# Kernel tuning notes

Hardware: AMD Instinct MI355X
Metric: run time of the kernel (lower is better)

The kernel has to match this reference:

```python
import jax, jax.numpy as jnp
import numpy as np

B, N, DIM = 1, 512, 1024
HEADS, DH = 16, 64          # dim_head = 64, _dim = heads*dh = 1024
P = 32                      # projection_dim
P2 = P // 2
NEG_INF = -1e30


def setup_inputs() -> dict:
    key = jax.random.key(0)
    ks = jax.random.split(key, 14)
    s = 0.02
    _dim = HEADS * DH
    return {
        "x":    jax.random.normal(ks[0], (B, N, DIM), dtype=jnp.float32),
        "Wqkv": jax.random.normal(ks[1], (3 * _dim, DIM), dtype=jnp.float32) * s,
        "Wout": jax.random.normal(ks[2], (DIM, _dim), dtype=jnp.float32) * s,
        "Wq":   jax.random.normal(ks[3], (P, DH), dtype=jnp.float32) * s,
        "bq":   jax.random.normal(ks[4], (P,), dtype=jnp.float32) * s,
        "Wk":   jax.random.normal(ks[5], (P, DH), dtype=jnp.float32) * s,
        "bk":   jax.random.normal(ks[6], (P,), dtype=jnp.float32) * s,
        "W1":   jax.random.normal(ks[7], (P, 2 * P), dtype=jnp.float32) * s,
        "b1":   jax.random.normal(ks[8], (P,), dtype=jnp.float32) * s,
        "W2":   jax.random.normal(ks[9], (P2, P), dtype=jnp.float32) * s,
        "b2":   jax.random.normal(ks[10], (P2,), dtype=jnp.float32) * s,
        "W3":   jax.random.normal(ks[11], (1, P2), dtype=jnp.float32) * s,
        "b3":   jax.random.normal(ks[12], (1,), dtype=jnp.float32) * s,
    }


def reference(x, Wqkv, Wout, Wq, bq, Wk, bk, W1, b1, W2, b2, W3, b3):
    b, n, _ = x.shape
    # qkv projection, then einops 'b n (d k h) -> k b h n d' split (d outermost!)
    qkv = jnp.einsum('bnc,oc->bno', x, Wqkv).reshape(b, n, DH, 3, HEADS)
    q = jnp.transpose(qkv[:, :, :, 0, :], (0, 3, 1, 2))  # [b,h,n,dh]
    k = jnp.transpose(qkv[:, :, :, 1, :], (0, 3, 1, 2))
    v = jnp.transpose(qkv[:, :, :, 2, :], (0, 3, 1, 2))

    qp = jnp.einsum('bhnd,pd->bhnp', q, Wq) + bq  # [b,h,n,P]
    kp = jnp.einsum('bhnd,pd->bhnp', k, Wk) + bk

    # linear1 on concat(q_i, k_j): split W1 -> broadcast-add (same math,
    # avoids materializing the [b,h,n,n,2P] concat tensor)
    W1q, W1k = W1[:, :P], W1[:, P:]
    a = jnp.einsum('bhnp,qp->bhnq', qp, W1q)      # [b,h,n,P]
    c = jnp.einsum('bhnp,qp->bhnq', kp, W1k)      # [b,h,n,P]
    h1 = jax.nn.relu(a[:, :, :, None, :] + c[:, :, None, :, :] + b1)  # [b,h,n,n,P]
    h2 = jax.nn.relu(jnp.einsum('bhijp,qp->bhijq', h1, W2) + b2)      # [b,h,n,n,P/2]
    score = jnp.einsum('bhijq,oq->bhijo', h2, W3)[..., 0] + b3[0]     # [b,h,n,n]

    # causal mask (triu(1) filled with -inf)
    i = jnp.arange(n)
    causal = i[None, :] > i[:, None]
    score = jnp.where(causal, NEG_INF, score)

    attn = jax.nn.softmax(score, axis=-1)
    out = jnp.einsum('bhij,bhjd->bhid', attn, v)                      # [b,h,n,dh]
    out = jnp.transpose(out, (0, 2, 1, 3)).reshape(b, n, HEADS * DH)  # b n (h d)
    return jnp.einsum('bne,oe->bno', out, Wout)
```

## Files before the change

### kernel.cpp

```cpp
#include <hip/hip_runtime.h>
#include <hip/hip_bf16.h>
#include <hip/hip_fp16.h>
#include <math.h>

#define N_SEQ 512
#define DIM   1024
#define HEADS 16
#define DH    64
#define P     32
#define P2    16
#define PSTR  520

typedef short    bf16x8 __attribute__((ext_vector_type(8)));
typedef _Float16 f16x8  __attribute__((ext_vector_type(8)));
typedef float    f32x4  __attribute__((ext_vector_type(4)));

__device__ inline unsigned short f2bf(float f) {
  union { float f; unsigned u; } v; v.f = f;
  unsigned r = (v.u + 0x7fffu + ((v.u >> 16) & 1u)) >> 16;
  return (unsigned short)r;
}

union H8 { f16x8 v; __half2 h2[4]; unsigned u32[4]; };

__global__ __launch_bounds__(256) void prep(
    const float* __restrict__ Wqkv, const float* __restrict__ Wq,
    const float* __restrict__ bq, const float* __restrict__ Wk,
    const float* __restrict__ bk, const float* __restrict__ W1,
    const float* __restrict__ x, const float* __restrict__ Wout,
    short* __restrict__ Wcomb, short* __restrict__ xb,
    short* __restrict__ Woutb, float* __restrict__ ba32,
    float* __restrict__ bc32) {
  const int b = blockIdx.x, tid = threadIdx.x;
  if (b < 256) {
    __shared__ float W1s[32][33];
    __shared__ float Wqs[32][65];
    __shared__ float wsm[32][65];
    __shared__ __align__(16) float qs[64][132];
    const int part = b >> 7, rem = b & 127;
    const int h = rem >> 3, c0 = (rem & 7) * 128;
    const int grow = part * 16 + h;
    for (int idx = tid; idx < 1024; idx += 256)
      W1s[idx >> 5][idx & 31] = W1[(idx >> 5) * 64 + part * 32 + (idx & 31)];
    const float* Wsel = part ? Wk : Wq;
    for (int idx = tid; idx < 2048; idx += 256)
      Wqs[idx >> 6][idx & 63] = Wsel[idx];
    for (int idx = tid; idx < 2048; idx += 256) {
      const int d = idx >> 5, c4 = idx & 31;
      *(float4*)&qs[d][c4 * 4] =
          *(const float4*)(Wqkv + (size_t)(d * 48 + grow) * DIM + c0 + c4 * 4);
    }
    __syncthreads();
    for (int idx = tid; idx < 2048; idx += 256) {
      const int q = idx >> 6, d = idx & 63;
      float s = 0.f;
#pragma unroll
      for (int p = 0; p < 32; ++p) s += W1s[q][p] * Wqs[p][d];
      wsm[q][d] = s;
    }
    __syncthreads();
    for (int idx = tid; idx < 4096; idx += 256) {
      const int q = idx >> 7, c = idx & 127;
      float s = 0.f;
#pragma unroll
      for (int d = 0; d < 64; ++d) s += wsm[q][d] * qs[d][c];
      Wcomb[(size_t)(part * 512 + h * 32 + q) * DIM + c0 + c] = (short)f2bf(s);
    }
    if (rem == 0 && tid < 32) {
      const float* bsel = part ? bk : bq;
      float s = 0.f;
#pragma unroll
      for (int p = 0; p < 32; ++p) s += W1s[tid][p] * bsel[p];
      (part ? bc32 : ba32)[tid] = s;
    }
  } else if (b < 384) {
#pragma unroll
    for (int rr = 0; rr < 8; ++rr) {
      const int ov = (b - 256) * 8 + rr;
      const int h = ov >> 6, d = ov & 63;
      const float4 v = *(const float4*)(Wqkv + (size_t)(d * 48 + 32 + h) * DIM + tid * 4);
      ushort4 o;
      o.x = f2bf(v.x); o.y = f2bf(v.y); o.z = f2bf(v.z); o.w = f2bf(v.w);
      *(ushort4*)(Wcomb + (size_t)(1024 + ov) * DIM + tid * 4) = o;
    }
  } else if (b < 512) {
    const int idx = (b - 384) * 256 + tid;
#pragma unroll
    for (int u = 0; u < 4; ++u) {
      const int t = u * 32768 + idx;
      const float4 v = ((const float4*)x)[t];
      ushort4 o;
      o.x = f2bf(v.x); o.y = f2bf(v.y); o.z = f2bf(v.z); o.w = f2bf(v.w);
      ((ushort4*)xb)[t] = o;
    }
  } else {
    const int idx = (b - 512) * 256 + tid;
#pragma unroll
    for (int u = 0; u < 4; ++u) {
      const int t = u * 65536 + idx;
      const float4 v = ((const float4*)Wout)[t];
      ushort4 o;
      o.x = f2bf(v.x); o.y = f2bf(v.y); o.z = f2bf(v.z); o.w = f2bf(v.w);
      ((ushort4*)Woutb)[t] = o;
    }
  }
}

__global__ __launch_bounds__(256) void gemm_acv(
    const short* __restrict__ xb, const short* __restrict__ Wcomb,
    const float* __restrict__ ba32, const float* __restrict__ bc32,
    const float* __restrict__ b1,
    __half* __restrict__ a_buf, __half* __restrict__ cb_buf,
    __half* __restrict__ vT) {
  const int wave = blockIdx.x * 4 + (threadIdx.x >> 6);
  const int tm = wave >> 6;
  const int tn = wave & 63;
  const int lane = threadIdx.x & 63;
  const int m = lane & 15;
  const int quad = lane >> 4;

  const short* pa  = xb + (size_t)(tm * 16 + m) * DIM + quad * 8;
  const short* pb0 = Wcomb + (size_t)(tn * 32 + m) * DIM + quad * 8;
  const short* pb1 = pb0 + (size_t)16 * DIM;

  f32x4 acc0 = {0.f,0.f,0.f,0.f}, acc1 = {0.f,0.f,0.f,0.f};
#pragma unroll 4
  for (int k = 0; k < DIM; k += 32) {
    const bf16x8 av = *(const bf16x8*)(pa + k);
    const bf16x8 b0 = *(const bf16x8*)(pb0 + k);
    const bf16x8 b1v = *(const bf16x8*)(pb1 + k);
    acc0 = __builtin_amdgcn_mfma_f32_16x16x32_bf16(av, b0, acc0, 0, 0, 0);
    acc1 = __builtin_amdgcn_mfma_f32_16x16x32_bf16(av, b1v, acc1, 0, 0, 0);
  }

#pragma unroll
  for (int r = 0; r < 4; ++r) {
    const int n = tm * 16 + quad * 4 + r;
#pragma unroll
    for (int half = 0; half < 2; ++half) {
      const int o = tn * 32 + m + half * 16;
      const float val = half ? acc1[r] : acc0[r];
      if (o < 512) {
        const int h = o >> 5, q = o & 31;
        a_buf[((size_t)h * N_SEQ + n) * P + q] = __float2half(val + ba32[q]);
      } else if (o < 1024) {
        const int oo = o - 512, h = oo >> 5, q = oo & 31;
        cb_buf[((size_t)h * N_SEQ + n) * P + q] = __float2half(val + bc32[q] + b1[q]);
      } else {
        const int ov = o - 1024, h = ov >> 6, d = ov & 63;
        vT[((size_t)h * DH + d) * N_SEQ + n] = __float2half(val);
      }
    }
  }
}

__device__ inline float rowscore(const H8& a, const H8& c, f16x8 w2f,
                                 float4 b2q, float4 w3q) {
  H8 u;
#pragma unroll
  for (int k = 0; k < 4; ++k) {
    const __half2 s = __hadd2(a.h2[k], c.h2[k]);
    union { __half2 h; unsigned u; } cv; cv.h = s;
    const unsigned msk = (cv.u >> 15) & 0x00010001u;
    u.u32[k] = cv.u & ~(msk * 0xFFFFu);
  }
  f32x4 acc = {0.f, 0.f, 0.f, 0.f};
  acc = __builtin_amdgcn_mfma_f32_16x16x32_f16(w2f, u.v, acc, 0, 0, 0);
  return fmaxf(acc[0] + b2q.x, 0.f) * w3q.x + fmaxf(acc[1] + b2q.y, 0.f) * w3q.y
       + fmaxf(acc[2] + b2q.z, 0.f) * w3q.z + fmaxf(acc[3] + b2q.w, 0.f) * w3q.w;
}

__device__ inline float quadreduce4(float p0, float p1, float p2, float p3,
                                    int quad) {
  const float sx = (quad & 1) ? p0 : p1;
  const float sy = (quad & 1) ? p2 : p3;
  const float rx = __shfl_xor(sx, 16);
  const float ry = __shfl_xor(sy, 16);
  const float aa = ((quad & 1) ? p1 : p0) + rx;
  const float bb = ((quad & 1) ? p3 : p2) + ry;
  const float sz = (quad & 2) ? aa : bb;
  const float rz = __shfl_xor(sz, 32);
  return ((quad & 2) ? bb : aa) + rz;
}

__global__ __launch_bounds__(256) void attn_fused(
    const __half* __restrict__ a_g, const __half* __restrict__ cb_g,
    const float* __restrict__ W2, const float* __restrict__ b2,
    const float* __restrict__ W3,
    const __half* __restrict__ vT, short* __restrict__ attnb) {
  const int p = blockIdx.x;
  const int h = blockIdx.y;
  const int tid = threadIdx.x;
  const int w = tid >> 6;
  const int lane = tid & 63;
  const int m = lane & 15, quad = lane >> 4;

  __shared__ __align__(16) __half probS[32][PSTR];
  __shared__ float invS[32];

  const int tlo = p, thi = 31 - p;
  const int nlo = p + 1, nhi = 32 - p;

  {
    f16x8 w2f;
    {
      const float4* wp = (const float4*)(W2 + m * P + quad * 8);
      const float4 w0 = wp[0], w1 = wp[1];
      H8 u;
      u.h2[0] = __floats2half2_rn(w0.x, w0.y);
      u.h2[1] = __floats2half2_rn(w0.z, w0.w);
      u.h2[2] = __floats2half2_rn(w1.x, w1.y);
      u.h2[3] = __floats2half2_rn(w1.z, w1.w);
      w2f = u.v;
    }
    const float4 b2q = *(const float4*)(b2 + quad * 4);
    const float4 w3q = *(const float4*)(W3 + quad * 4);

    H8 alo[4], ahi[4];
#pragma unroll
    for (int r = 0; r < 4; ++r) {
      alo[r].v = *(const f16x8*)(a_g + ((size_t)h * N_SEQ + tlo * 16 + 4 * w + r) * P + quad * 8);
      ahi[r].v = *(const f16x8*)(a_g + ((size_t)h * N_SEQ + thi * 16 + 4 * w + r) * P + quad * 8);
    }

    for (int jt = 0; jt < nhi; ++jt) {
      H8 cb;
      cb.v = *(const f16x8*)(cb_g + ((size_t)h * N_SEQ + jt * 16 + m) * P + quad * 8);
      const float q0 = rowscore(ahi[0], cb, w2f, b2q, w3q);
      const float q1 = rowscore(ahi[1], cb, w2f, b2q, w3q);
      const float q2 = rowscore(ahi[2], cb, w2f, b2q, w3q);
      const float q3 = rowscore(ahi[3], cb, w2f, b2q, w3q);
      const float fh = quadreduce4(q0, q1, q2, q3, quad);
      probS[16 + 4 * w + quad][jt * 16 + m] = __float2half(fh);
      if (jt < nlo) {
        const float s0 = rowscore(alo[0], cb, w2f, b2q, w3q);
        const float s1 = rowscore(alo[1], cb, w2f, b2q, w3q);
        const float s2 = rowscore(alo[2], cb, w2f, b2q, w3q);
        const float s3 = rowscore(alo[3], cb, w2f, b2q, w3q);
        const float fl = quadreduce4(s0, s1, s2, s3, quad);
        probS[4 * w + quad][jt * 16 + m] = __float2half(fl);
      }
    }
  }
  __syncthreads();

  {
    const int lr = 8 * w + (lane >> 3);
    const int c  = lane & 7;
    const int gi = (lr < 16) ? (tlo * 16 + lr) : (thi * 16 + (lr - 16));
    float mx = -1e30f;
#pragma unroll
    for (int k = 0; k < 8; ++k) {
      const int c0 = k * 64 + c * 8;
      if (c0 > gi) break;
      H8 vv; vv.v = *(const f16x8*)&probS[lr][c0];
#pragma unroll
      for (int u = 0; u < 8; ++u) {
        const float s = __half2float(vv.h2[u >> 1].data[u & 1]);
        if (c0 + u <= gi) mx = fmaxf(mx, s);
      }
    }
#pragma unroll
    for (int msk = 1; msk < 8; msk <<= 1) mx = fmaxf(mx, __shfl_xor(mx, msk));
    float sum = 0.f;
#pragma unroll
    for (int k = 0; k < 8; ++k) {
      const int c0 = k * 64 + c * 8;
      H8 vv; vv.v = *(const f16x8*)&probS[lr][c0];
      H8 o;
#pragma unroll
      for (int u = 0; u < 4; ++u) {
        float e0 = 0.f, e1 = 0.f;
        if (c0 + 2 * u <= gi) {
          e0 = __expf(__half2float(vv.h2[u].data[0]) - mx);
          if (c0 + 2 * u + 1 <= gi)
            e1 = __expf(__half2float(vv.h2[u].data[1]) - mx);
        }
        sum += e0 + e1;
        o.h2[u] = __floats2half2_rn(e0, e1);
      }
      *(f16x8*)&probS[lr][c0] = o.v;
    }
#pragma unroll
    for (int msk = 1; msk < 8; msk <<= 1) sum += __shfl_xor(sum, msk);
    if (c == 0) invS[lr] = 1.f / sum;
  }
  __syncthreads();

  {
    const int d0 = w * 16;
    const __half* pb = vT + ((size_t)h * DH + d0 + m) * N_SEQ + quad * 8;
#pragma unroll
    for (int half = 0; half < 2; ++half) {
      const int lbase = half ? 16 : 0;
      const int tile = half ? thi : tlo;
      const int nk = half ? ((33 - p) >> 1) : ((p + 2) >> 1);
      f32x4 acc = {0.f, 0.f, 0.f, 0.f};
      for (int k = 0; k < nk; ++k) {
        const f16x8 a = *(const f16x8*)&probS[lbase + m][k * 32 + quad * 8];
        const f16x8 b = *(const f16x8*)(pb + k * 32);
        acc = __builtin_amdgcn_mfma_f32_16x16x32_f16(a, b, acc, 0, 0, 0);
      }
#pragma unroll
      for (int r = 0; r < 4; ++r) {
        const int lrow = quad * 4 + r;
        const float val = acc[r] * invS[lbase + lrow];
        attnb[(size_t)(tile * 16 + lrow) * DIM + h * DH + d0 + m] = (short)f2bf(val);
      }
    }
  }
}

__global__ __launch_bounds__(256) void gemm_out16(
    const short* __restrict__ A, const short* __restrict__ B,
    float* __restrict__ C) {
  const int wave = blockIdx.x * 4 + (threadIdx.x >> 6);
  const int tm = wave >> 6;
  const int tn = wave & 63;
  const int lane = threadIdx.x & 63;
  const int m = lane & 15, quad = lane >> 4;

  const short* pa = A + (size_t)(tm * 16 + m) * DIM + quad * 8;
  const short* pb = B + (size_t)(tn * 16 + m) * DIM + quad * 8;

  f32x4 acc = {0.f, 0.f, 0.f, 0.f};
#pragma unroll 4
  for (int k = 0; k < DIM; k += 32) {
    const bf16x8 a = *(const bf16x8*)(pa + k);
    const bf16x8 b = *(const bf16x8*)(pb + k);
    acc = __builtin_amdgcn_mfma_f32_16x16x32_bf16(a, b, acc, 0, 0, 0);
  }
#pragma unroll
  for (int r = 0; r < 4; ++r)
    C[(size_t)(tm * 16 + quad * 4 + r) * DIM + tn * 16 + m] = acc[r];
}

extern "C" void kernel_launch(void* const* d_in, const int* in_sizes, int n_in,
                              void* d_out, int out_size, void* d_ws, size_t ws_size,
                              hipStream_t stream) {
  const float* x    = (const float*)d_in[0];
  const float* Wqkv = (const float*)d_in[1];
  const float* Wout = (const float*)d_in[2];
  const float* Wq   = (const float*)d_in[3];
  const float* bq   = (const float*)d_in[4];
  const float* Wk   = (const float*)d_in[5];
  const float* bk   = (const float*)d_in[6];
  const float* W1   = (const float*)d_in[7];
  const float* b1   = (const float*)d_in[8];
  const float* W2   = (const float*)d_in[9];
  const float* b2   = (const float*)d_in[10];
  const float* W3   = (const float*)d_in[11];
  float* out = (float*)d_out;

  float*  ws     = (float*)d_ws;
  float*  ba32   = ws;
  float*  bc32   = ba32 + 32;
  __half* a_buf  = (__half*)(bc32 + 32);
  __half* cb_buf = a_buf + (size_t)HEADS * N_SEQ * P;
  __half* vT     = cb_buf + (size_t)HEADS * N_SEQ * P;
  short*  Wcomb  = (short*)(vT + (size_t)HEADS * DH * N_SEQ);
  short*  xb     = Wcomb + (size_t)2048 * DIM;
  short*  Woutb  = xb + (size_t)N_SEQ * DIM;
  short*  attnb  = Woutb + (size_t)DIM * DIM;

  prep<<<768, 256, 0, stream>>>(Wqkv, Wq, bq, Wk, bk, W1, x, Wout,
                                Wcomb, xb, Woutb, ba32, bc32);

  gemm_acv<<<512, 256, 0, stream>>>(xb, Wcomb, ba32, bc32, b1,
                                    a_buf, cb_buf, vT);

  dim3 g3(16, HEADS);
  attn_fused<<<g3, 256, 0, stream>>>(a_buf, cb_buf, W2, b2, W3, vT, attnb);

  gemm_out16<<<512, 256, 0, stream>>>(attnb, Woutb, out);
}
```

Before: 174.8 us.

## Register-block GEMMs to 128x128 tiles, double attention block threads, simplify rowscore

Both bf16 GEMMs switch from one 16x16/16x32 tile per wave to 64x64 register-blocked tiles per wave in 128x128 blocks. Each loaded fragment now feeds four MFMAs, cutting global load traffic per MFMA, but the grids shrink to 64 and 32 blocks on a GPU with many CUs. The attention kernel moves to 512 threads, splitting score tiles by parity across wave pairs and giving each wave a single PV half, which adds parallelism per block. Rowscore replaces the bitmask ReLU with a vector max, folds b2 into the MFMA accumulator init, and b1 is folded into bc32 during prep.

```diff
diff --git a/kernel.cpp b/kernel.cpp
--- a/kernel.cpp
+++ b/kernel.cpp
@@ -27,6 +27,7 @@
     const float* __restrict__ Wqkv, const float* __restrict__ Wq,
     const float* __restrict__ bq, const float* __restrict__ Wk,
     const float* __restrict__ bk, const float* __restrict__ W1,
+    const float* __restrict__ b1,
     const float* __restrict__ x, const float* __restrict__ Wout,
     short* __restrict__ Wcomb, short* __restrict__ xb,
     short* __restrict__ Woutb, float* __restrict__ ba32,
@@ -71,6 +72,7 @@
       float s = 0.f;
 #pragma unroll
       for (int p = 0; p < 32; ++p) s += W1s[tid][p] * bsel[p];
+      if (part) s += b1[tid];
       (part ? bc32 : ba32)[tid] = s;
     }
   } else if (b < 384) {
@@ -109,65 +111,76 @@
 __global__ __launch_bounds__(256) void gemm_acv(
     const short* __restrict__ xb, const short* __restrict__ Wcomb,
     const float* __restrict__ ba32, const float* __restrict__ bc32,
-    const float* __restrict__ b1,
     __half* __restrict__ a_buf, __half* __restrict__ cb_buf,
     __half* __restrict__ vT) {
-  const int wave = blockIdx.x * 4 + (threadIdx.x >> 6);
-  const int tm = wave >> 6;
-  const int tn = wave & 63;
+  const int bb = blockIdx.x;
+  const int tm = bb >> 4;
+  const int tn = bb & 15;
+  const int w = threadIdx.x >> 6;
+  const int wm = w >> 1, wn = w & 1;
   const int lane = threadIdx.x & 63;
-  const int m = lane & 15;
-  const int quad = lane >> 4;
-
-  const short* pa  = xb + (size_t)(tm * 16 + m) * DIM + quad * 8;
-  const short* pb0 = Wcomb + (size_t)(tn * 32 + m) * DIM + quad * 8;
-  const short* pb1 = pb0 + (size_t)16 * DIM;
-
-  f32x4 acc0 = {0.f,0.f,0.f,0.f}, acc1 = {0.f,0.f,0.f,0.f};
-#pragma unroll 4
+  const int m = lane & 15, quad = lane >> 4;
+
+  const int row0 = tm * 128 + wm * 64;
+  const int col0 = tn * 128 + wn * 64;
+
+  const short* pa = xb + (size_t)(row0 + m) * DIM + quad * 8;
+  const short* pb = Wcomb + (size_t)(col0 + m) * DIM + quad * 8;
+
+  f32x4 acc[4][4];
+#pragma unroll
+  for (int mi = 0; mi < 4; ++mi)
+#pragma unroll
+    for (int ni = 0; ni < 4; ++ni) acc[mi][ni] = (f32x4){0.f, 0.f, 0.f, 0.f};
+
+#pragma unroll 2
   for (int k = 0; k < DIM; k += 32) {
-    const bf16x8 av = *(const bf16x8*)(pa + k);
-    const bf16x8 b0 = *(const bf16x8*)(pb0 + k);
-    const bf16x8 b1v = *(const bf16x8*)(pb1 + k);
-    acc0 = __builtin_amdgcn_mfma_f32_16x16x32_bf16(av, b0, acc0, 0, 0, 0);
-    acc1 = __builtin_amdgcn_mfma_f32_16x16x32_bf16(av, b1v, acc1, 0, 0, 0);
-  }
-
-#pragma unroll
-  for (int r = 0; r < 4; ++r) {
-    const int n = tm * 16 + quad * 4 + r;
-#pragma unroll
-    for (int half = 0; half < 2; ++half) {
-      const int o = tn * 32 + m + half * 16;
-      const float val = half ? acc1[r] : acc0[r];
-      if (o < 512) {
-        const int h = o >> 5, q = o & 31;
-        a_buf[((size_t)h * N_SEQ + n) * P + q] = __float2half(val + ba32[q]);
-      } else if (o < 1024) {
-        const int oo = o - 512, h = oo >> 5, q = oo & 31;
-        cb_buf[((size_t)h * N_SEQ + n) * P + q] = __float2half(val + bc32[q] + b1[q]);
-      } else {
-        const int ov = o - 1024, h = ov >> 6, d = ov & 63;
-        vT[((size_t)h * DH + d) * N_SEQ + n] = __float2half(val);
+    bf16x8 af[4], bf[4];
+#pragma unroll
+    for (int i = 0; i < 4; ++i) {
+      af[i] = *(const bf16x8*)(pa + (size_t)i * 16 * DIM + k);
+      bf[i] = *(const bf16x8*)(pb + (size_t)i * 16 * DIM + k);
+    }
+#pragma unroll
+    for (int mi = 0; mi < 4; ++mi)
+#pragma unroll
+      for (int ni = 0; ni < 4; ++ni)
+        acc[mi][ni] = __builtin_amdgcn_mfma_f32_16x16x32_bf16(
+            af[mi], bf[ni], acc[mi][ni], 0, 0, 0);
+  }
+
+#pragma unroll
+  for (int mi = 0; mi < 4; ++mi) {
+#pragma unroll
+    for (int ni = 0; ni < 4; ++ni) {
+      const int o = col0 + ni * 16 + m;
+#pragma unroll
+      for (int r = 0; r < 4; ++r) {
+        const int n = row0 + mi * 16 + quad * 4 + r;
+        const float val = acc[mi][ni][r];
+        if (o < 512) {
+          const int hh = o >> 5, q = o & 31;
+          a_buf[((size_t)hh * N_SEQ + n) * P + q] = __float2half(val + ba32[q]);
+        } else if (o < 1024) {
+          const int oo = o - 512, hh = oo >> 5, q = oo & 31;
+          cb_buf[((size_t)hh * N_SEQ + n) * P + q] = __float2half(val + bc32[q]);
+        } else {
+          const int ov = o - 1024, hh = ov >> 6, d = ov & 63;
+          vT[((size_t)hh * DH + d) * N_SEQ + n] = __float2half(val);
+        }
       }
     }
   }
 }
 
 __device__ inline float rowscore(const H8& a, const H8& c, f16x8 w2f,
-                                 float4 b2q, float4 w3q) {
-  H8 u;
-#pragma unroll
-  for (int k = 0; k < 4; ++k) {
-    const __half2 s = __hadd2(a.h2[k], c.h2[k]);
-    union { __half2 h; unsigned u; } cv; cv.h = s;
-    const unsigned msk = (cv.u >> 15) & 0x00010001u;
-    u.u32[k] = cv.u & ~(msk * 0xFFFFu);
-  }
-  f32x4 acc = {0.f, 0.f, 0.f, 0.f};
-  acc = __builtin_amdgcn_mfma_f32_16x16x32_f16(w2f, u.v, acc, 0, 0, 0);
-  return fmaxf(acc[0] + b2q.x, 0.f) * w3q.x + fmaxf(acc[1] + b2q.y, 0.f) * w3q.y
-       + fmaxf(acc[2] + b2q.z, 0.f) * w3q.z + fmaxf(acc[3] + b2q.w, 0.f) * w3q.w;
+                                 f32x4 b2q, float4 w3q) {
+  const f16x8 z = (f16x8)(_Float16)0;
+  const f16x8 u = __builtin_elementwise_max(a.v + c.v, z);
+  f32x4 acc = b2q;
+  acc = __builtin_amdgcn_mfma_f32_16x16x32_f16(w2f, u, acc, 0, 0, 0);
+  return fmaxf(acc[0], 0.f) * w3q.x + fmaxf(acc[1], 0.f) * w3q.y
+       + fmaxf(acc[2], 0.f) * w3q.z + fmaxf(acc[3], 0.f) * w3q.w;
 }
 
 __device__ inline float quadreduce4(float p0, float p1, float p2, float p3,
@@ -183,7 +196,7 @@
   return ((quad & 2) ? bb : aa) + rz;
 }
 
-__global__ __launch_bounds__(256) void attn_fused(
+__global__ __launch_bounds__(512) void attn_fused(
     const __half* __restrict__ a_g, const __half* __restrict__ cb_g,
     const float* __restrict__ W2, const float* __restrict__ b2,
     const float* __restrict__ W3,
@@ -202,28 +215,31 @@
   const int nlo = p + 1, nhi = 32 - p;
 
   {
+    const int g = w & 3;
+    const int par = w >> 2;
     f16x8 w2f;
     {
       const float4* wp = (const float4*)(W2 + m * P + quad * 8);
       const float4 w0 = wp[0], w1 = wp[1];
-      H8 u;
-      u.h2[0] = __floats2half2_rn(w0.x, w0.y);
-      u.h2[1] = __floats2half2_rn(w0.z, w0.w);
-      u.h2[2] = __floats2half2_rn(w1.x, w1.y);
-      u.h2[3] = __floats2half2_rn(w1.z, w1.w);
-      w2f = u.v;
-    }
-    const float4 b2q = *(const float4*)(b2 + quad * 4);
+      H8 uu;
+      uu.h2[0] = __floats2half2_rn(w0.x, w0.y);
+      uu.h2[1] = __floats2half2_rn(w0.z, w0.w);
+      uu.h2[2] = __floats2half2_rn(w1.x, w1.y);
+      uu.h2[3] = __floats2half2_rn(w1.z, w1.w);
+      w2f = uu.v;
+    }
+    const float4 b2f = *(const float4*)(b2 + quad * 4);
+    const f32x4 b2q = {b2f.x, b2f.y, b2f.z, b2f.w};
     const float4 w3q = *(const float4*)(W3 + quad * 4);
 
     H8 alo[4], ahi[4];
 #pragma unroll
     for (int r = 0; r < 4; ++r) {
-      alo[r].v = *(const f16x8*)(a_g + ((size_t)h * N_SEQ + tlo * 16 + 4 * w + r) * P + quad * 8);
-      ahi[r].v = *(const f16x8*)(a_g + ((size_t)h * N_SEQ + thi * 16 + 4 * w + r) * P + quad * 8);
-    }
-
-    for (int jt = 0; jt < nhi; ++jt) {
+      alo[r].v = *(const f16x8*)(a_g + ((size_t)h * N_SEQ + tlo * 16 + 4 * g + r) * P + quad * 8);
+      ahi[r].v = *(const f16x8*)(a_g + ((size_t)h * N_SEQ + thi * 16 + 4 * g + r) * P + quad * 8);
+    }
+
+    for (int jt = par; jt < nhi; jt += 2) {
       H8 cb;
       cb.v = *(const f16x8*)(cb_g + ((size_t)h * N_SEQ + jt * 16 + m) * P + quad * 8);
       const float q0 = rowscore(ahi[0], cb, w2f, b2q, w3q);
@@ -231,82 +247,80 @@
       const float q2 = rowscore(ahi[2], cb, w2f, b2q, w3q);
       const float q3 = rowscore(ahi[3], cb, w2f, b2q, w3q);
       const float fh = quadreduce4(q0, q1, q2, q3, quad);
-      probS[16 + 4 * w + quad][jt * 16 + m] = __float2half(fh);
+      probS[16 + 4 * g + quad][jt * 16 + m] = __float2half(fh);
       if (jt < nlo) {
         const float s0 = rowscore(alo[0], cb, w2f, b2q, w3q);
         const float s1 = rowscore(alo[1], cb, w2f, b2q, w3q);
         const float s2 = rowscore(alo[2], cb, w2f, b2q, w3q);
         const float s3 = rowscore(alo[3], cb, w2f, b2q, w3q);
         const float fl = quadreduce4(s0, s1, s2, s3, quad);
-        probS[4 * w + quad][jt * 16 + m] = __float2half(fl);
+        probS[4 * g + quad][jt * 16 + m] = __float2half(fl);
       }
     }
   }
   __syncthreads();
 
   {
-    const int lr = 8 * w + (lane >> 3);
-    const int c  = lane & 7;
+    const int lr = tid >> 4;
+    const int c  = tid & 15;
     const int gi = (lr < 16) ? (tlo * 16 + lr) : (thi * 16 + (lr - 16));
     float mx = -1e30f;
 #pragma unroll
-    for (int k = 0; k < 8; ++k) {
-      const int c0 = k * 64 + c * 8;
+    for (int k = 0; k < 4; ++k) {
+      const int c0 = k * 128 + c * 8;
       if (c0 > gi) break;
       H8 vv; vv.v = *(const f16x8*)&probS[lr][c0];
 #pragma unroll
-      for (int u = 0; u < 8; ++u) {
-        const float s = __half2float(vv.h2[u >> 1].data[u & 1]);
-        if (c0 + u <= gi) mx = fmaxf(mx, s);
+      for (int uu = 0; uu < 8; ++uu) {
+        const float s = __half2float(vv.h2[uu >> 1].data[uu & 1]);
+        if (c0 + uu <= gi) mx = fmaxf(mx, s);
       }
     }
 #pragma unroll
-    for (int msk = 1; msk < 8; msk <<= 1) mx = fmaxf(mx, __shfl_xor(mx, msk));
+    for (int msk = 1; msk < 16; msk <<= 1) mx = fmaxf(mx, __shfl_xor(mx, msk));
     float sum = 0.f;
 #pragma unroll
-    for (int k = 0; k < 8; ++k) {
-      const int c0 = k * 64 + c * 8;
+    for (int k = 0; k < 4; ++k) {
+      const int c0 = k * 128 + c * 8;
       H8 vv; vv.v = *(const f16x8*)&probS[lr][c0];
       H8 o;
 #pragma unroll
-      for (int u = 0; u < 4; ++u) {
+      for (int uu = 0; uu < 4; ++uu) {
         float e0 = 0.f, e1 = 0.f;
-        if (c0 + 2 * u <= gi) {
-          e0 = __expf(__half2float(vv.h2[u].data[0]) - mx);
-          if (c0 + 2 * u + 1 <= gi)
-            e1 = __expf(__half2float(vv.h2[u].data[1]) - mx);
+        if (c0 + 2 * uu <= gi) {
+          e0 = __expf(__half2float(vv.h2[uu].data[0]) - mx);
+          if (c0 + 2 * uu + 1 <= gi)
+            e1 = __expf(__half2float(vv.h2[uu].data[1]) - mx);
         }
         sum += e0 + e1;
-        o.h2[u] = __floats2half2_rn(e0, e1);
+        o.h2[uu] = __floats2half2_rn(e0, e1);
       }
       *(f16x8*)&probS[lr][c0] = o.v;
     }
 #pragma unroll
-    for (int msk = 1; msk < 8; msk <<= 1) sum += __shfl_xor(sum, msk);
+    for (int msk = 1; msk < 16; msk <<= 1) sum += __shfl_xor(sum, msk);
     if (c == 0) invS[lr] = 1.f / sum;
   }
   __syncthreads();
 
   {
-    const int d0 = w * 16;
+    const int half = w >> 2;
+    const int d0 = (w & 3) * 16;
     const __half* pb = vT + ((size_t)h * DH + d0 + m) * N_SEQ + quad * 8;
-#pragma unroll
-    for (int half = 0; half < 2; ++half) {
-      const int lbase = half ? 16 : 0;
-      const int tile = half ? thi : tlo;
-      const int nk = half ? ((33 - p) >> 1) : ((p + 2) >> 1);
-      f32x4 acc = {0.f, 0.f, 0.f, 0.f};
-      for (int k = 0; k < nk; ++k) {
-        const f16x8 a = *(const f16x8*)&probS[lbase + m][k * 32 + quad * 8];
-        const f16x8 b = *(const f16x8*)(pb + k * 32);
-        acc = __builtin_amdgcn_mfma_f32_16x16x32_f16(a, b, acc, 0, 0, 0);
-      }
-#pragma unroll
-      for (int r = 0; r < 4; ++r) {
-        const int lrow = quad * 4 + r;
-        const float val = acc[r] * invS[lbase + lrow];
-        attnb[(size_t)(tile * 16 + lrow) * DIM + h * DH + d0 + m] = (short)f2bf(val);
-      }
+    const int lbase = half ? 16 : 0;
+    const int tile = half ? thi : tlo;
+    const int nk = half ? ((33 - p) >> 1) : ((p + 2) >> 1);
+    f32x4 acc = {0.f, 0.f, 0.f, 0.f};
+    for (int k = 0; k < nk; ++k) {
+      const f16x8 aa = *(const f16x8*)&probS[lbase + m][k * 32 + quad * 8];
+      const f16x8 bb = *(const f16x8*)(pb + k * 32);
+      acc = __builtin_amdgcn_mfma_f32_16x16x32_f16(aa, bb, acc, 0, 0, 0);
+    }
+#pragma unroll
+    for (int r = 0; r < 4; ++r) {
+      const int lrow = quad * 4 + r;
+      const float val = acc[r] * invS[lbase + lrow];
+      attnb[(size_t)(tile * 16 + lrow) * DIM + h * DH + d0 + m] = (short)f2bf(val);
     }
   }
 }
@@ -314,25 +328,53 @@
 __global__ __launch_bounds__(256) void gemm_out16(
     const short* __restrict__ A, const short* __restrict__ B,
     float* __restrict__ C) {
-  const int wave = blockIdx.x * 4 + (threadIdx.x >> 6);
-  const int tm = wave >> 6;
-  const int tn = wave & 63;
+  const int bb = blockIdx.x;
+  const int tm = bb >> 3;
+  const int tn = bb & 7;
+  const int w = threadIdx.x >> 6;
+  const int wm = w >> 1, wn = w & 1;
   const int lane = threadIdx.x & 63;
   const int m = lane & 15, quad = lane >> 4;
 
-  const short* pa = A + (size_t)(tm * 16 + m) * DIM + quad * 8;
-  const short* pb = B + (size_t)(tn * 16 + m) * DIM + quad * 8;
-
-  f32x4 acc = {0.f, 0.f, 0.f, 0.f};
-#pragma unroll 4
+  const int row0 = tm * 128 + wm * 64;
+  const int col0 = tn * 128 + wn * 64;
+
+  const short* pa = A + (size_t)(row0 + m) * DIM + quad * 8;
+  const short* pb = B + (size_t)(col0 + m) * DIM + quad * 8;
+
+  f32x4 acc[4][4];
+#pragma unroll
+  for (int mi = 0; mi < 4; ++mi)
+#pragma unroll
+    for (int ni = 0; ni < 4; ++ni) acc[mi][ni] = (f32x4){0.f, 0.f, 0.f, 0.f};
+
+#pragma unroll 2
   for (int k = 0; k < DIM; k += 32) {
-    const bf16x8 a = *(const bf16x8*)(pa + k);
-    const bf16x8 b = *(const bf16x8*)(pb + k);
-    acc = __builtin_amdgcn_mfma_f32_16x16x32_bf16(a, b, acc, 0, 0, 0);
-  }
-#pragma unroll
-  for (int r = 0; r < 4; ++r)
-    C[(size_t)(tm * 16 + quad * 4 + r) * DIM + tn * 16 + m] = acc[r];
+    bf16x8 af[4], bf[4];
+#pragma unroll
+    for (int i = 0; i < 4; ++i) {
+      af[i] = *(const bf16x8*)(pa + (size_t)i * 16 * DIM + k);
+      bf[i] = *(const bf16x8*)(pb + (size_t)i * 16 * DIM + k);
+    }
+#pragma unroll
+    for (int mi = 0; mi < 4; ++mi)
+#pragma unroll
+      for (int ni = 0; ni < 4; ++ni)
+        acc[mi][ni] = __builtin_amdgcn_mfma_f32_16x16x32_bf16(
+            af[mi], bf[ni], acc[mi][ni], 0, 0, 0);
+  }
+
+#pragma unroll
+  for (int mi = 0; mi < 4; ++mi)
+#pragma unroll
+    for (int ni = 0; ni < 4; ++ni) {
+      const int o = col0 + ni * 16 + m;
+#pragma unroll
+      for (int r = 0; r < 4; ++r) {
+        const int n = row0 + mi * 16 + quad * 4 + r;
+        C[(size_t)n * DIM + o] = acc[mi][ni][r];
+      }
+    }
 }
 
 extern "C" void kernel_launch(void* const* d_in, const int* in_sizes, int n_in,
@@ -363,14 +405,13 @@
   short*  Woutb  = xb + (size_t)N_SEQ * DIM;
   short*  attnb  = Woutb + (size_t)DIM * DIM;
 
-  prep<<<768, 256, 0, stream>>>(Wqkv, Wq, bq, Wk, bk, W1, x, Wout,
+  prep<<<768, 256, 0, stream>>>(Wqkv, Wq, bq, Wk, bk, W1, b1, x, Wout,
                                 Wcomb, xb, Woutb, ba32, bc32);
 
-  gemm_acv<<<512, 256, 0, stream>>>(xb, Wcomb, ba32, bc32, b1,
-                                    a_buf, cb_buf, vT);
+  gemm_acv<<<64, 256, 0, stream>>>(xb, Wcomb, ba32, bc32, a_buf, cb_buf, vT);
 
   dim3 g3(16, HEADS);
-  attn_fused<<<g3, 256, 0, stream>>>(a_buf, cb_buf, W2, b2, W3, vT, attnb);
-
-  gemm_out16<<<512, 256, 0, stream>>>(attnb, Woutb, out);
-}
+  attn_fused<<<g3, 512, 0, stream>>>(a_buf, cb_buf, W2, b2, W3, vT, attnb);
+
+  gemm_out16<<<32, 256, 0, stream>>>(attnb, Woutb, out);
+}
```

Result: slower. 199.5 us (+14.1%).
